# Kernel tuning notes

Hardware: AMD Instinct MI355X
Metric: run time of the kernel (lower is better)

## Reference

```python
import jax, jax.numpy as jnp
import numpy as np

OUT_H = 512
OUT_W = 512
GRID_SIZE = 3
N = GRID_SIZE * GRID_SIZE  # number of TPS control points
BATCH = 32


def setup_inputs() -> dict:
    key = jax.random.key(0)
    # theta = [Q_X (N), Q_Y (N), P_X (N), P_Y (N)]
    theta = jax.random.normal(key, (BATCH, 4 * N), dtype=jnp.float32)
    return {"theta": theta}


def _compute_L_inverse(PX, PY):
    # PX, PY: [B, N] control point coordinates
    d2 = (PX[:, :, None] - PX[:, None, :]) ** 2 + (PY[:, :, None] - PY[:, None, :]) ** 2
    d2 = jnp.where(d2 == 0, 1.0, d2)
    K = d2 * jnp.log(d2)                                        # [B, N, N]
    O = jnp.ones((PX.shape[0], N, 1), dtype=PX.dtype)
    P = jnp.concatenate([O, PX[:, :, None], PY[:, :, None]], axis=2)  # [B, N, 3]
    Z = jnp.zeros((PX.shape[0], 3, 3), dtype=PX.dtype)
    L = jnp.concatenate([
        jnp.concatenate([K, P], axis=2),
        jnp.concatenate([jnp.swapaxes(P, 1, 2), Z], axis=2),
    ], axis=1)                                                  # [B, N+3, N+3]
    return jnp.linalg.inv(L)


def reference(theta):
    # theta: [B, 4N]
    QX = theta[:, :N]
    QY = theta[:, N:2 * N]
    PX = theta[:, 2 * N:3 * N]
    PY = theta[:, 3 * N:]

    Li = _compute_L_inverse(PX, PY)                             # [B, N+3, N+3]
    WX = jnp.einsum('bij,bj->bi', Li[:, :N, :N], QX)            # [B, N]
    WY = jnp.einsum('bij,bj->bi', Li[:, :N, :N], QY)
    AX = jnp.einsum('bij,bj->bi', Li[:, N:, :N], QX)            # [B, 3]
    AY = jnp.einsum('bij,bj->bi', Li[:, N:, :N], QY)

    gx = jnp.linspace(-1.0, 1.0, OUT_W, dtype=theta.dtype)
    gy = jnp.linspace(-1.0, 1.0, OUT_H, dtype=theta.dtype)
    GX, GY = jnp.meshgrid(gx, gy)                               # [H, W]

    # squared distances from every pixel to every control point: [B, H, W, N]
    d2 = (GX[None, :, :, None] - PX[:, None, None, :]) ** 2 \
       + (GY[None, :, :, None] - PY[:, None, None, :]) ** 2
    d2 = jnp.where(d2 == 0, 1.0, d2)
    U = d2 * jnp.log(d2)

    xp = (AX[:, 0, None, None]
          + AX[:, 1, None, None] * GX[None]
          + AX[:, 2, None, None] * GY[None]
          + jnp.einsum('bhwn,bn->bhw', U, WX))                  # [B, H, W]
    yp = (AY[:, 0, None, None]
          + AY[:, 1, None, None] * GX[None]
          + AY[:, 2, None, None] * GY[None]
          + jnp.einsum('bhwn,bn->bhw', U, WY))

    return jnp.stack([xp, yp], axis=-1)                         # [B, H, W, 2]
```

## Files before the change

kernel.cpp:

```cpp
#include <hip/hip_runtime.h>
#include <math.h>

#define NCTRL 9
#define DIM 12
#define NCOLS (DIM + 2)
#define OUT_H 512
#define OUT_W 512
#define BATCH 32

__global__ __launch_bounds__(64) void tps_solve_kernel(
    const float* __restrict__ theta, float* __restrict__ coef) {
    const int b = blockIdx.x;
    const int lane = threadIdx.x;
    const float* th = theta + b * 36;

    __shared__ double M[DIM][NCOLS + 1];
    __shared__ double fshare[DIM];

    for (int e = lane; e < DIM * NCOLS; e += 64) {
        const int r = e / NCOLS;
        const int c = e % NCOLS;
        double v;
        if (c < DIM) {
            if (r < NCTRL && c < NCTRL) {
                const double dx = (double)th[18 + r] - (double)th[18 + c];
                const double dy = (double)th[27 + r] - (double)th[27 + c];
                const double d2 = dx * dx + dy * dy;
                v = (d2 == 0.0) ? 0.0 : d2 * log(d2);
            } else if (r < NCTRL) {
                v = (c == 9) ? 1.0 : (c == 10 ? (double)th[18 + r] : (double)th[27 + r]);
            } else if (c < NCTRL) {
                v = (r == 9) ? 1.0 : (r == 10 ? (double)th[18 + c] : (double)th[27 + c]);
            } else {
                v = 0.0;
            }
        } else if (c == DIM) {
            v = (r < NCTRL) ? (double)th[r] : 0.0;
        } else {
            v = (r < NCTRL) ? (double)th[9 + r] : 0.0;
        }
        M[r][c] = v;
    }
    __syncthreads();

    for (int k = 0; k < DIM; ++k) {
        double mv = (lane >= k && lane < DIM) ? fabs(M[lane][k]) : -1.0;
        int mi = lane;
        #pragma unroll
        for (int off = 32; off > 0; off >>= 1) {
            const double ov = __shfl_xor(mv, off);
            const int oi = __shfl_xor(mi, off);
            if (ov > mv) { mv = ov; mi = oi; }
        }
        mi = __shfl(mi, 0);
        if (mi != k && lane < NCOLS) {
            const double tmp = M[k][lane];
            M[k][lane] = M[mi][lane];
            M[mi][lane] = tmp;
        }
        __syncthreads();

        const double piv = M[k][k];
        if (lane < DIM && lane != k) fshare[lane] = M[lane][k] / piv;
        __syncthreads();

        for (int e = lane; e < DIM * NCOLS; e += 64) {
            const int r = e / NCOLS;
            const int c = e % NCOLS;
            if (r != k && c >= k) M[r][c] -= fshare[r] * M[k][c];
        }
        __syncthreads();
    }

    if (lane < DIM) {
        const double x = M[lane][DIM] / M[lane][lane];
        const double y = M[lane][DIM + 1] / M[lane][lane];
        float* cb = coef + b * 24;
        if (lane < NCTRL) {
            cb[lane] = (float)x;
            cb[9 + lane] = (float)y;
        } else {
            cb[18 + (lane - 9)] = (float)x;
            cb[21 + (lane - 9)] = (float)y;
        }
    }
}

__global__ __launch_bounds__(256) void tps_grid_kernel(
    const float* __restrict__ theta, const float* __restrict__ coef,
    float* __restrict__ out) {
    const int b = blockIdx.y;
    const float* th = theta + b * 36;
    const float* cf = coef + b * 24;

    float PX[NCTRL], PY[NCTRL], WX[NCTRL], WY[NCTRL];
    #pragma unroll
    for (int n = 0; n < NCTRL; ++n) {
        PX[n] = th[18 + n];
        PY[n] = th[27 + n];
        WX[n] = cf[n];
        WY[n] = cf[9 + n];
    }
    const float AX0 = cf[18], AX1 = cf[19], AX2 = cf[20];
    const float AY0 = cf[21], AY1 = cf[22], AY2 = cf[23];

    const int p = blockIdx.x * 256 + threadIdx.x;
    const int pix = p * 2;
    const int w = pix & (OUT_W - 1);
    const int h = pix >> 9;

    const float step = 2.0f / 511.0f;
    const float gx0 = -1.0f + step * (float)w;
    const float gx1 = gx0 + step;
    const float gy = -1.0f + step * (float)h;

    float xp0 = AX0 + AX1 * gx0 + AX2 * gy;
    float yp0 = AY0 + AY1 * gx0 + AY2 * gy;
    float xp1 = AX0 + AX1 * gx1 + AX2 * gy;
    float yp1 = AY0 + AY1 * gx1 + AY2 * gy;

    #pragma unroll
    for (int n = 0; n < NCTRL; ++n) {
        const float dy = gy - PY[n];
        const float dy2 = dy * dy;

        const float dx0 = gx0 - PX[n];
        const float r20 = dx0 * dx0 + dy2;
        const float u0 = (r20 == 0.0f) ? 0.0f : r20 * __logf(r20);

        const float dx1 = gx1 - PX[n];
        const float r21 = dx1 * dx1 + dy2;
        const float u1 = (r21 == 0.0f) ? 0.0f : r21 * __logf(r21);

        xp0 += u0 * WX[n];
        yp0 += u0 * WY[n];
        xp1 += u1 * WX[n];
        yp1 += u1 * WY[n];
    }

    const size_t off = ((size_t)b * (OUT_H * OUT_W) + (size_t)pix) * 2;
    float4 o;
    o.x = xp0; o.y = yp0; o.z = xp1; o.w = yp1;
    *(float4*)(out + off) = o;
}

extern "C" void kernel_launch(void* const* d_in, const int* in_sizes, int n_in,
                              void* d_out, int out_size, void* d_ws, size_t ws_size,
                              hipStream_t stream) {
    const float* theta = (const float*)d_in[0];
    float* out = (float*)d_out;
    float* coef = (float*)d_ws;

    tps_solve_kernel<<<dim3(BATCH), dim3(64), 0, stream>>>(theta, coef);

    const int pairs_per_batch = (OUT_H * OUT_W) / 2;
    const int blocks_x = pairs_per_batch / 256;
    tps_grid_kernel<<<dim3(blocks_x, BATCH), dim3(256), 0, stream>>>(theta, coef, out);
}
```

Before: 114.3 us.

## Compute four pixels per thread with nontemporal stores and branchless log

The grid kernel now computes four adjacent pixels per thread instead of two. It steps dx incrementally, replaces the zero-distance branch with a clamp inside the log, and writes results with two nontemporal float4 stores. The solve kernel's pivot-search shuffle reduction is shortened to 16 lanes, since only 12 rows exist. The aim is to amortise per-thread setup, cut instruction count and keep the large output write from polluting the cache, at the cost of half as many threads and more registers per thread. The incremental dx may drift slightly from the per-pixel gx computation.

```diff
diff --git a/kernel.cpp b/kernel.cpp
--- a/kernel.cpp
+++ b/kernel.cpp
@@ -7,6 +7,8 @@
 #define OUT_H 512
 #define OUT_W 512
 #define BATCH 32
+
+typedef float nfloat4 __attribute__((ext_vector_type(4)));
 
 __global__ __launch_bounds__(64) void tps_solve_kernel(
     const float* __restrict__ theta, float* __restrict__ coef) {
@@ -47,7 +49,7 @@
         double mv = (lane >= k && lane < DIM) ? fabs(M[lane][k]) : -1.0;
         int mi = lane;
         #pragma unroll
-        for (int off = 32; off > 0; off >>= 1) {
+        for (int off = 8; off > 0; off >>= 1) {
             const double ov = __shfl_xor(mv, off);
             const int oi = __shfl_xor(mi, off);
             if (ov > mv) { mv = ov; mi = oi; }
@@ -105,43 +107,42 @@
     const float AY0 = cf[21], AY1 = cf[22], AY2 = cf[23];
 
     const int p = blockIdx.x * 256 + threadIdx.x;
-    const int pix = p * 2;
+    const int pix = p * 4;
     const int w = pix & (OUT_W - 1);
     const int h = pix >> 9;
 
     const float step = 2.0f / 511.0f;
     const float gx0 = -1.0f + step * (float)w;
-    const float gx1 = gx0 + step;
     const float gy = -1.0f + step * (float)h;
 
-    float xp0 = AX0 + AX1 * gx0 + AX2 * gy;
-    float yp0 = AY0 + AY1 * gx0 + AY2 * gy;
-    float xp1 = AX0 + AX1 * gx1 + AX2 * gy;
-    float yp1 = AY0 + AY1 * gx1 + AY2 * gy;
+    float xp[4], yp[4];
+    #pragma unroll
+    for (int i = 0; i < 4; ++i) {
+        const float gx = gx0 + step * (float)i;
+        xp[i] = AX0 + AX1 * gx + AX2 * gy;
+        yp[i] = AY0 + AY1 * gx + AY2 * gy;
+    }
 
     #pragma unroll
     for (int n = 0; n < NCTRL; ++n) {
         const float dy = gy - PY[n];
         const float dy2 = dy * dy;
-
-        const float dx0 = gx0 - PX[n];
-        const float r20 = dx0 * dx0 + dy2;
-        const float u0 = (r20 == 0.0f) ? 0.0f : r20 * __logf(r20);
-
-        const float dx1 = gx1 - PX[n];
-        const float r21 = dx1 * dx1 + dy2;
-        const float u1 = (r21 == 0.0f) ? 0.0f : r21 * __logf(r21);
-
-        xp0 += u0 * WX[n];
-        yp0 += u0 * WY[n];
-        xp1 += u1 * WX[n];
-        yp1 += u1 * WY[n];
+        float dx = gx0 - PX[n];
+        #pragma unroll
+        for (int i = 0; i < 4; ++i) {
+            const float r2 = __builtin_fmaf(dx, dx, dy2);
+            const float u = r2 * __logf(fmaxf(r2, 1e-30f));
+            xp[i] = __builtin_fmaf(u, WX[n], xp[i]);
+            yp[i] = __builtin_fmaf(u, WY[n], yp[i]);
+            dx += step;
+        }
     }
 
     const size_t off = ((size_t)b * (OUT_H * OUT_W) + (size_t)pix) * 2;
-    float4 o;
-    o.x = xp0; o.y = yp0; o.z = xp1; o.w = yp1;
-    *(float4*)(out + off) = o;
+    nfloat4 o0 = {xp[0], yp[0], xp[1], yp[1]};
+    nfloat4 o1 = {xp[2], yp[2], xp[3], yp[3]};
+    __builtin_nontemporal_store(o0, (nfloat4*)(out + off));
+    __builtin_nontemporal_store(o1, (nfloat4*)(out + off + 4));
 }
 
 extern "C" void kernel_launch(void* const* d_in, const int* in_sizes, int n_in,
@@ -153,7 +154,7 @@
 
     tps_solve_kernel<<<dim3(BATCH), dim3(64), 0, stream>>>(theta, coef);
 
-    const int pairs_per_batch = (OUT_H * OUT_W) / 2;
-    const int blocks_x = pairs_per_batch / 256;
+    const int quads_per_batch = (OUT_H * OUT_W) / 4;
+    const int blocks_x = quads_per_batch / 256;
     tps_grid_kernel<<<dim3(blocks_x, BATCH), dim3(256), 0, stream>>>(theta, coef, out);
 }
```

Measured after the change: 110.4 us. 1.04x faster.
